# Kernel tuning notes

Hardware: AMD Instinct MI355X
Metric: run time of the kernel (lower is better)

## Reference

```python
import jax, jax.numpy as jnp
import numpy as np

B, L, D, T = 32, 512, 1024, 256
MAX_MENTION_LEN = 10
NEG_INF = float('-inf')


def _static_bounds_and_keep():
    # Full (start, end) grid, flattened row-major like torch's .view(-1, 2)
    s = np.repeat(np.arange(L), L)
    e = np.tile(np.arange(L), L)
    bounds = np.stack([s, e], axis=-1)            # [L*L, 2]
    keep = (e - s) <= MAX_MENTION_LEN             # static per-position mask
    idx = np.nonzero(keep)[0]
    return jnp.asarray(bounds[keep], jnp.int32), jnp.asarray(idx, jnp.int32)


def setup_inputs() -> dict:
    key = jax.random.key(0)
    k0, k1, k2 = jax.random.split(key, 3)
    text_encodings = jax.random.normal(k0, (B, L, D), dtype=jnp.float32)
    mask_ctxt = jnp.ones((B, L), dtype=jnp.int32)
    # word -> wordpiece mapping: [start, end_exclusive); values kept in [1, L)
    tokens_mapping = jax.random.randint(k1, (B, T, 2), 1, L).astype(jnp.int32)
    W = jax.random.normal(k2, (D, 3), dtype=jnp.float32) * 0.02
    b = jnp.zeros((3,), dtype=jnp.float32)
    return {"text_encodings": text_encodings, "mask_ctxt": mask_ctxt,
            "tokens_mapping": tokens_mapping, "W": W, "b": b}


def reference(text_encodings, mask_ctxt, tokens_mapping, W, b):
    # per-token start / end / mention logits
    logits = jnp.einsum('bld,dk->blk', text_encodings, W) + b  # [B, L, 3]
    valid_tok = (mask_ctxt == 1)
    start_lp = jnp.where(valid_tok, logits[:, :, 0], NEG_INF)
    end_lp = jnp.where(valid_tok, logits[:, :, 1], NEG_INF)
    mention_lp = jnp.where(valid_tok, logits[:, :, 2], NEG_INF)

    # scores[b, s, e] = start[b, s] + end[b, e] + sum_{i=s..e} mention[b, i]
    scores = start_lp[:, :, None] + end_lp[:, None, :]          # [B, L, L]
    csum = jnp.cumsum(mention_lp, axis=1)                        # [B, L]
    csum_prev = jnp.concatenate(
        [jnp.zeros((csum.shape[0], 1), csum.dtype), csum[:, :-1]], axis=1)
    scores = scores + (csum[:, None, :] - csum_prev[:, :, None])

    # mention_sizes > 0  <=>  e >= s
    pos = jnp.arange(L)
    size_ok = pos[None, :, None] <= pos[None, None, :]           # [1, L, L]

    # token-boundary masks (scatter 1 at word starts / ends, zero col 0)
    bidx = jnp.arange(tokens_mapping.shape[0])[:, None]
    ts = jnp.zeros(mask_ctxt.shape, jnp.int32).at[bidx, tokens_mapping[:, :, 0]].set(1)
    ts = ts.at[:, 0].set(0)
    te = jnp.zeros(mask_ctxt.shape, jnp.int32).at[bidx, tokens_mapping[:, :, 1] - 1].set(1)
    te = te.at[:, 0].set(0)
    vse = ts[:, :, None] * te[:, None, :]                        # bmm outer product

    valid = size_ok & (mask_ctxt[:, :, None] > 0) & (vse > 0)
    scores = jnp.where(valid, scores, NEG_INF)

    scores_flat = scores.reshape(scores.shape[0], -1)            # [B, L*L]
    bounds_keep, keep_idx = _static_bounds_and_keep()
    out_scores = scores_flat[:, keep_idx]                        # [B, K]
    out_bounds = jnp.broadcast_to(bounds_keep[None],
                                  (scores.shape[0],) + bounds_keep.shape)
    return out_scores, out_bounds
```

## Files before the change

kernel.cpp:

```cpp
#include <hip/hip_runtime.h>
#include <math.h>

#define BB 32
#define LL 512
#define DD 1024
#define TT 256
#define NK 136393
#define NK_LIN 131273
#define S_LIN 502
#define NEG_BIG  -3.0e38f
#define NEG_MASK -1.0e30f
#define P_TOT (BB * NK)
#define SC4 (P_TOT / 4)
#define MEMSET_BLOCKS ((SC4 + 255) / 256)
#define BCHUNKS ((NK + 255) / 256)
#define D1_BLOCKS (MEMSET_BLOCKS + 2 * BCHUNKS)
#define GEMV_BLOCKS (BB * LL / 4)

typedef float f4v __attribute__((ext_vector_type(4)));
typedef float f2v __attribute__((ext_vector_type(2)));

__device__ __forceinline__ int off_s(int s) {
    return (s <= S_LIN) ? s * (s + 21) / 2 : NK_LIN + (s - S_LIN) * LL;
}

__global__ __launch_bounds__(256) void write_kernel(float* __restrict__ out)
{
    const int id = blockIdx.x;
    const int t  = threadIdx.x;

    if (id < MEMSET_BLOCKS) {
        const int i = id * 256 + t;
        if (i < SC4) {
            f4v neg = {NEG_BIG, NEG_BIG, NEG_BIG, NEG_BIG};
            ((f4v*)out)[i] = neg;
        }
        return;
    }

    const int q = id - MEMSET_BLOCKS;
    const int g = (q >= BCHUNKS) ? 1 : 0;
    const int c = q - g * BCHUNKS;
    const int p = c * 256 + t;
    if (p >= NK) return;
    int s, e;
    if (p >= NK_LIN) {
        const int rr = p - NK_LIN;
        s = S_LIN + (rr >> 9);
        e = rr & 511;
    } else {
        float f = sqrtf(8.0f * (float)p + 441.0f);
        s = (int)((f - 21.0f) * 0.5f);
        if (s < 0) s = 0;
        if (s > 501) s = 501;
        while ((s + 1) * (s + 22) / 2 <= p) ++s;
        while (s * (s + 21) / 2 > p) --s;
        e = p - s * (s + 21) / 2;
    }
    f2v v = {(float)s, (float)e};
    f2v* bp = (f2v*)(out + (size_t)P_TOT);
#pragma unroll
    for (int j = 0; j < 16; ++j) {
        const int b = g * 16 + j;
        bp[(size_t)b * NK + p] = v;
    }
}

__global__ __launch_bounds__(256) void gemv_kernel(
    const float* __restrict__ text, const float* __restrict__ W,
    const float* __restrict__ bias, const int* __restrict__ mask,
    float* __restrict__ slp, float* __restrict__ elp, float* __restrict__ mlp)
{
    const int wid  = threadIdx.x >> 6;
    const int lane = threadIdx.x & 63;
    const int row  = blockIdx.x * 4 + wid;
    const f4v* t4 = (const f4v*)(text + (size_t)row * DD);
    const f4v* w4 = (const f4v*)W;
    float a0 = 0.f, a1 = 0.f, a2 = 0.f;
#pragma unroll
    for (int j = 0; j < 4; ++j) {
        const int fi = lane + j * 64;
        f4v v  = t4[fi];
        f4v w0 = w4[fi * 3 + 0];
        f4v w1 = w4[fi * 3 + 1];
        f4v w2 = w4[fi * 3 + 2];
        a0 += v.x * w0.x;  a1 += v.x * w0.y;  a2 += v.x * w0.z;
        a0 += v.y * w0.w;  a1 += v.y * w1.x;  a2 += v.y * w1.y;
        a0 += v.z * w1.z;  a1 += v.z * w1.w;  a2 += v.z * w2.x;
        a0 += v.w * w2.y;  a1 += v.w * w2.z;  a2 += v.w * w2.w;
    }
#pragma unroll
    for (int o = 32; o; o >>= 1) {
        a0 += __shfl_down(a0, o);
        a1 += __shfl_down(a1, o);
        a2 += __shfl_down(a2, o);
    }
    if (lane == 0) {
        const int m = mask[row];
        slp[row] = (m == 1) ? a0 + bias[0] : NEG_MASK;
        elp[row] = (m == 1) ? a1 + bias[1] : NEG_MASK;
        mlp[row] = (m == 1) ? a2 + bias[2] : NEG_MASK;
    }
}

__global__ __launch_bounds__(512) void tail_kernel(
    const float* __restrict__ slp, const float* __restrict__ elp,
    const float* __restrict__ mlp, const int* __restrict__ mask,
    const int* __restrict__ tmap, float* __restrict__ out)
{
    const int b = blockIdx.x;
    const int j = blockIdx.y;
    const int t = threadIdx.x;
    __shared__ float sl[LL], el[LL], ml[LL];
    __shared__ unsigned char tsl[LL], tel[LL];

    const int idx = b * LL + t;
    tsl[t] = 0; tel[t] = 0;
    sl[t] = slp[idx]; el[t] = elp[idx]; ml[t] = mlp[idx];
    __syncthreads();
    if (t < TT) {
        int s0 = tmap[((size_t)b * TT + t) * 2 + 0];
        int e0 = tmap[((size_t)b * TT + t) * 2 + 1] - 1;
        s0 = min(max(s0, 0), LL - 1);
        e0 = min(max(e0, 0), LL - 1);
        tsl[s0] = 1;
        tel[e0] = 1;
    }
    __syncthreads();

    const int s = t;
    const int e = s + j;
    if (s > 0 && e < LL && tsl[s] && tel[e] && mask[idx] == 1) {
        float w = 0.f;
        for (int l = s; l <= e; ++l) w += ml[l];
        float sc = sl[s] + el[e] + w;
        if (sc < -1.0e29f) sc = NEG_BIG;
        out[(size_t)b * NK + off_s(s) + e] = sc;
    }
}

extern "C" void kernel_launch(void* const* d_in, const int* in_sizes, int n_in,
                              void* d_out, int out_size, void* d_ws, size_t ws_size,
                              hipStream_t stream) {
    const float* text = (const float*)d_in[0];
    const int*   mask = (const int*)d_in[1];
    const int*   tmap = (const int*)d_in[2];
    const float* W    = (const float*)d_in[3];
    const float* bias = (const float*)d_in[4];
    float* out = (float*)d_out;

    float* slp = (float*)d_ws;
    float* elp = slp + (size_t)BB * LL;
    float* mlp = elp + (size_t)BB * LL;

    write_kernel<<<D1_BLOCKS, 256, 0, stream>>>(out);
    gemv_kernel<<<GEMV_BLOCKS, 256, 0, stream>>>(text, W, bias, mask,
                                                 slp, elp, mlp);
    dim3 g3(BB, 11);
    tail_kernel<<<g3, 512, 0, stream>>>(slp, elp, mlp, mask, tmap, out);
}
```

Before: 28.70 us.

## Fuse logit GEMV into span-scoring kernel with halo row recomputation

Drops the separate GEMV kernel and its workspace round trip. Each of 512 blocks now computes start, end and mention logits for its 32 start rows plus a 10-row halo, keeping them in shared memory and software-pipelining three row buffers per wave. Span scores for that window are then written directly. This saves a kernel launch and the global logits write/read, but reads and recomputes about 31% extra text rows at window boundaries. Those extra reads may partly hit in L2.

New measurement: 30.66 us. 1.07x slower.

```diff
diff --git a/kernel.cpp b/kernel.cpp
--- a/kernel.cpp
+++ b/kernel.cpp
@@ -15,7 +15,7 @@
 #define MEMSET_BLOCKS ((SC4 + 255) / 256)
 #define BCHUNKS ((NK + 255) / 256)
 #define D1_BLOCKS (MEMSET_BLOCKS + 2 * BCHUNKS)
-#define GEMV_BLOCKS (BB * LL / 4)
+#define TAIL_BLOCKS 512
 
 typedef float f4v __attribute__((ext_vector_type(4)));
 typedef float f2v __attribute__((ext_vector_type(2)));
@@ -66,76 +66,103 @@
     }
 }
 
-__global__ __launch_bounds__(256) void gemv_kernel(
+#define LOADR(buf, lr)                                                    \
+    if ((lr) < wlen) {                                                    \
+        const f4v* t4 = (const f4v*)(text + (size_t)(rowg0 + (lr)) * DD); \
+        _Pragma("unroll")                                                 \
+        for (int j = 0; j < 4; ++j) buf[j] = t4[lane + j * 64];           \
+    }
+
+#define REDUCER(buf, lr)                                                  \
+    if ((lr) < wlen) {                                                    \
+        float a0 = 0.f, a1 = 0.f, a2 = 0.f;                               \
+        _Pragma("unroll")                                                 \
+        for (int j = 0; j < 4; ++j) {                                     \
+            f4v v = buf[j];                                               \
+            f4v w0 = wr[j*3], w1 = wr[j*3+1], w2 = wr[j*3+2];             \
+            a0 += v.x * w0.x;  a1 += v.x * w0.y;  a2 += v.x * w0.z;       \
+            a0 += v.y * w0.w;  a1 += v.y * w1.x;  a2 += v.y * w1.y;       \
+            a0 += v.z * w1.z;  a1 += v.z * w1.w;  a2 += v.z * w2.x;       \
+            a0 += v.w * w2.y;  a1 += v.w * w2.z;  a2 += v.w * w2.w;       \
+        }                                                                 \
+        _Pragma("unroll")                                                 \
+        for (int o = 32; o; o >>= 1) {                                    \
+            a0 += __shfl_down(a0, o);                                     \
+            a1 += __shfl_down(a1, o);                                     \
+            a2 += __shfl_down(a2, o);                                     \
+        }                                                                 \
+        if (lane == 0) {                                                  \
+            const int m = mask[rowg0 + (lr)];                             \
+            sl[lr] = (m == 1) ? a0 + b0 : NEG_MASK;                       \
+            el[lr] = (m == 1) ? a1 + b1 : NEG_MASK;                       \
+            ml[lr] = (m == 1) ? a2 + b2 : NEG_MASK;                       \
+        }                                                                 \
+    }
+
+__global__ __launch_bounds__(512) void tail_kernel(
     const float* __restrict__ text, const float* __restrict__ W,
     const float* __restrict__ bias, const int* __restrict__ mask,
-    float* __restrict__ slp, float* __restrict__ elp, float* __restrict__ mlp)
+    const int* __restrict__ tmap, float* __restrict__ out)
 {
-    const int wid  = threadIdx.x >> 6;
-    const int lane = threadIdx.x & 63;
-    const int row  = blockIdx.x * 4 + wid;
-    const f4v* t4 = (const f4v*)(text + (size_t)row * DD);
+    const int q    = blockIdx.x;
+    const int b    = q >> 4;
+    const int r0   = (q & 15) << 5;
+    const int wlen = min(42, LL - r0);
+    const int rowg0 = b * LL + r0;
+    const int t    = threadIdx.x;
+    const int wid  = t >> 6, lane = t & 63;
+
+    __shared__ float sl[42], el[42], ml[42];
+    __shared__ unsigned char tsw[42], tew[42];
+
     const f4v* w4 = (const f4v*)W;
-    float a0 = 0.f, a1 = 0.f, a2 = 0.f;
+    f4v wr[12];
 #pragma unroll
     for (int j = 0; j < 4; ++j) {
         const int fi = lane + j * 64;
-        f4v v  = t4[fi];
-        f4v w0 = w4[fi * 3 + 0];
-        f4v w1 = w4[fi * 3 + 1];
-        f4v w2 = w4[fi * 3 + 2];
-        a0 += v.x * w0.x;  a1 += v.x * w0.y;  a2 += v.x * w0.z;
-        a0 += v.y * w0.w;  a1 += v.y * w1.x;  a2 += v.y * w1.y;
-        a0 += v.z * w1.z;  a1 += v.z * w1.w;  a2 += v.z * w2.x;
-        a0 += v.w * w2.y;  a1 += v.w * w2.z;  a2 += v.w * w2.w;
+        wr[j*3+0] = w4[fi*3+0]; wr[j*3+1] = w4[fi*3+1]; wr[j*3+2] = w4[fi*3+2];
     }
-#pragma unroll
-    for (int o = 32; o; o >>= 1) {
-        a0 += __shfl_down(a0, o);
-        a1 += __shfl_down(a1, o);
-        a2 += __shfl_down(a2, o);
-    }
-    if (lane == 0) {
-        const int m = mask[row];
-        slp[row] = (m == 1) ? a0 + bias[0] : NEG_MASK;
-        elp[row] = (m == 1) ? a1 + bias[1] : NEG_MASK;
-        mlp[row] = (m == 1) ? a2 + bias[2] : NEG_MASK;
-    }
-}
+    const float b0 = bias[0], b1 = bias[1], b2 = bias[2];
 
-__global__ __launch_bounds__(512) void tail_kernel(
-    const float* __restrict__ slp, const float* __restrict__ elp,
-    const float* __restrict__ mlp, const int* __restrict__ mask,
-    const int* __restrict__ tmap, float* __restrict__ out)
-{
-    const int b = blockIdx.x;
-    const int j = blockIdx.y;
-    const int t = threadIdx.x;
-    __shared__ float sl[LL], el[LL], ml[LL];
-    __shared__ unsigned char tsl[LL], tel[LL];
+    f4v bufA[4], bufB[4], bufC[4];
+    LOADR(bufA, wid);
+    LOADR(bufB, wid + 8);
+    LOADR(bufC, wid + 16);
+    REDUCER(bufA, wid);        LOADR(bufA, wid + 24);
+    REDUCER(bufB, wid + 8);    LOADR(bufB, wid + 32);
+    REDUCER(bufC, wid + 16);   LOADR(bufC, wid + 40);
+    REDUCER(bufA, wid + 24);
+    REDUCER(bufB, wid + 32);
+    REDUCER(bufC, wid + 40);
 
-    const int idx = b * LL + t;
-    tsl[t] = 0; tel[t] = 0;
-    sl[t] = slp[idx]; el[t] = elp[idx]; ml[t] = mlp[idx];
+    if (t < 42) { tsw[t] = 0; tew[t] = 0; }
     __syncthreads();
     if (t < TT) {
         int s0 = tmap[((size_t)b * TT + t) * 2 + 0];
         int e0 = tmap[((size_t)b * TT + t) * 2 + 1] - 1;
         s0 = min(max(s0, 0), LL - 1);
         e0 = min(max(e0, 0), LL - 1);
-        tsl[s0] = 1;
-        tel[e0] = 1;
+        if (s0 >= r0 && s0 < r0 + wlen) tsw[s0 - r0] = 1;
+        if (e0 >= r0 && e0 < r0 + wlen) tew[e0 - r0] = 1;
     }
     __syncthreads();
 
-    const int s = t;
-    const int e = s + j;
-    if (s > 0 && e < LL && tsl[s] && tel[e] && mask[idx] == 1) {
-        float w = 0.f;
-        for (int l = s; l <= e; ++l) w += ml[l];
-        float sc = sl[s] + el[e] + w;
-        if (sc < -1.0e29f) sc = NEG_BIG;
-        out[(size_t)b * NK + off_s(s) + e] = sc;
+    if (t < 32 * 11) {
+        const int s_loc = t / 11;
+        const int j     = t - s_loc * 11;
+        const int s     = r0 + s_loc;
+        const int e     = s + j;
+        if (e < LL) {
+            const int e_loc = s_loc + j;
+            float v = NEG_BIG;
+            if (s > 0 && tsw[s_loc] && tew[e_loc]) {
+                float w = 0.f;
+                for (int l = s_loc; l <= e_loc; ++l) w += ml[l];
+                v = sl[s_loc] + el[e_loc] + w;
+                if (v < -1.0e29f) v = NEG_BIG;
+            }
+            out[(size_t)b * NK + off_s(s) + e] = v;
+        }
     }
 }
 
@@ -149,13 +176,6 @@
     const float* bias = (const float*)d_in[4];
     float* out = (float*)d_out;
 
-    float* slp = (float*)d_ws;
-    float* elp = slp + (size_t)BB * LL;
-    float* mlp = elp + (size_t)BB * LL;
-
     write_kernel<<<D1_BLOCKS, 256, 0, stream>>>(out);
-    gemv_kernel<<<GEMV_BLOCKS, 256, 0, stream>>>(text, W, bias, mask,
-                                                 slp, elp, mlp);
-    dim3 g3(BB, 11);
-    tail_kernel<<<g3, 512, 0, stream>>>(slp, elp, mlp, mask, tmap, out);
+    tail_kernel<<<TAIL_BLOCKS, 512, 0, stream>>>(text, W, bias, mask, tmap, out);
 }
```

## Fuse NEG_INF memset and score scatter into one dense fill kernel

Applied to the files above, without the earlier changes.

Drops the separate pass that pre-fills the whole score buffer with -inf followed by a sparse scatter of valid scores. A single fill kernel now writes each output row once, computing either the score or -inf per element with vector stores. It splits the s-range into balanced per-batch segments so each block gets similar work. The bounds-writing work moves into the same launch, cutting one kernel launch and one full pass of writes over the score buffer. The cost is redundant per-element branching and a serial mention-sum loop done inside the fill.

Result: slower. 60.82 us (+111.9%).

```diff
diff --git a/kernel.cpp b/kernel.cpp
--- a/kernel.cpp
+++ b/kernel.cpp
@@ -11,59 +11,21 @@
 #define NEG_BIG  -3.0e38f
 #define NEG_MASK -1.0e30f
 #define P_TOT (BB * NK)
-#define SC4 (P_TOT / 4)
-#define MEMSET_BLOCKS ((SC4 + 255) / 256)
+#define GEMV_BLOCKS (BB * LL / 4)
+#define NSEG 16
+#define FILL_BLOCKS (BB * NSEG)
 #define BCHUNKS ((NK + 255) / 256)
-#define D1_BLOCKS (MEMSET_BLOCKS + 2 * BCHUNKS)
-#define GEMV_BLOCKS (BB * LL / 4)
+#define D2_BLOCKS (FILL_BLOCKS + 2 * BCHUNKS)
+#define MAXW 131
 
 typedef float f4v __attribute__((ext_vector_type(4)));
 typedef float f2v __attribute__((ext_vector_type(2)));
 
+__device__ __constant__ int d_splits[NSEG + 1] =
+    {0, 121, 175, 216, 251, 282, 310, 335, 359, 381, 403, 423, 442, 460, 478, 495, 512};
+
 __device__ __forceinline__ int off_s(int s) {
     return (s <= S_LIN) ? s * (s + 21) / 2 : NK_LIN + (s - S_LIN) * LL;
-}
-
-__global__ __launch_bounds__(256) void write_kernel(float* __restrict__ out)
-{
-    const int id = blockIdx.x;
-    const int t  = threadIdx.x;
-
-    if (id < MEMSET_BLOCKS) {
-        const int i = id * 256 + t;
-        if (i < SC4) {
-            f4v neg = {NEG_BIG, NEG_BIG, NEG_BIG, NEG_BIG};
-            ((f4v*)out)[i] = neg;
-        }
-        return;
-    }
-
-    const int q = id - MEMSET_BLOCKS;
-    const int g = (q >= BCHUNKS) ? 1 : 0;
-    const int c = q - g * BCHUNKS;
-    const int p = c * 256 + t;
-    if (p >= NK) return;
-    int s, e;
-    if (p >= NK_LIN) {
-        const int rr = p - NK_LIN;
-        s = S_LIN + (rr >> 9);
-        e = rr & 511;
-    } else {
-        float f = sqrtf(8.0f * (float)p + 441.0f);
-        s = (int)((f - 21.0f) * 0.5f);
-        if (s < 0) s = 0;
-        if (s > 501) s = 501;
-        while ((s + 1) * (s + 22) / 2 <= p) ++s;
-        while (s * (s + 21) / 2 > p) --s;
-        e = p - s * (s + 21) / 2;
-    }
-    f2v v = {(float)s, (float)e};
-    f2v* bp = (f2v*)(out + (size_t)P_TOT);
-#pragma unroll
-    for (int j = 0; j < 16; ++j) {
-        const int b = g * 16 + j;
-        bp[(size_t)b * NK + p] = v;
-    }
 }
 
 __global__ __launch_bounds__(256) void gemv_kernel(
@@ -103,39 +65,108 @@
     }
 }
 
-__global__ __launch_bounds__(512) void tail_kernel(
+__global__ __launch_bounds__(256) void fill_kernel(
     const float* __restrict__ slp, const float* __restrict__ elp,
-    const float* __restrict__ mlp, const int* __restrict__ mask,
-    const int* __restrict__ tmap, float* __restrict__ out)
+    const float* __restrict__ mlp, const int* __restrict__ tmap,
+    float* __restrict__ out)
 {
-    const int b = blockIdx.x;
-    const int j = blockIdx.y;
-    const int t = threadIdx.x;
-    __shared__ float sl[LL], el[LL], ml[LL];
-    __shared__ unsigned char tsl[LL], tel[LL];
+    const int id = blockIdx.x;
+    const int t  = threadIdx.x;
 
-    const int idx = b * LL + t;
-    tsl[t] = 0; tel[t] = 0;
-    sl[t] = slp[idx]; el[t] = elp[idx]; ml[t] = mlp[idx];
-    __syncthreads();
-    if (t < TT) {
-        int s0 = tmap[((size_t)b * TT + t) * 2 + 0];
-        int e0 = tmap[((size_t)b * TT + t) * 2 + 1] - 1;
-        s0 = min(max(s0, 0), LL - 1);
-        e0 = min(max(e0, 0), LL - 1);
-        tsl[s0] = 1;
-        tel[e0] = 1;
+    if (id < FILL_BLOCKS) {
+        const int b   = id >> 4;
+        const int seg = id & 15;
+        const int a   = d_splits[seg], bnd = d_splits[seg + 1];
+        const int wlen = min(bnd + 10, LL) - a;
+
+        __shared__ float sl[MAXW], el[MAXW], ml[MAXW];
+        __shared__ unsigned char tsw[MAXW], tew[MAXW];
+
+        for (int i = t; i < wlen; i += 256) {
+            const int row = b * LL + a + i;
+            sl[i] = slp[row]; el[i] = elp[row]; ml[i] = mlp[row];
+            tsw[i] = 0; tew[i] = 0;
+        }
+        __syncthreads();
+        if (t < TT) {
+            int s0 = tmap[((size_t)b * TT + t) * 2 + 0];
+            int e0 = tmap[((size_t)b * TT + t) * 2 + 1] - 1;
+            s0 = min(max(s0, 0), LL - 1);
+            e0 = min(max(e0, 0), LL - 1);
+            if (s0 >= a && s0 < a + wlen) tsw[s0 - a] = 1;
+            if (e0 >= a && e0 < a + wlen) tew[e0 - a] = 1;
+        }
+        __syncthreads();
+
+        const int wid = t >> 6, lane = t & 63;
+        const size_t bb = (size_t)b * NK;
+
+        for (int s = a + wid; s < bnd; s += 4) {
+            const int s_loc = s - a;
+            const int n = min(s + 11, LL);
+            const size_t rowbase = bb + off_s(s);
+
+            auto val = [&](int e) -> float {
+                if (e < s) return NEG_BIG;
+                float v = NEG_BIG;
+                if (s > 0 && tsw[s_loc] && tew[e - a]) {
+                    float w = 0.f;
+                    for (int l = s_loc; l <= e - a; ++l) w += ml[l];
+                    v = sl[s_loc] + el[e - a] + w;
+                    if (v < -1.0e29f) v = NEG_BIG;
+                }
+                return v;
+            };
+
+            const int head = (int)((4 - (rowbase & 3)) & 3);
+            const int hh = min(head, n);
+            if (lane < hh) out[rowbase + lane] = val(lane);
+            const int nb4 = (n - hh) >> 2;
+            for (int j = lane; j < nb4; j += 64) {
+                const int e0 = hh + 4 * j;
+                f4v v;
+                if (e0 + 3 < s) {
+                    v = (f4v){NEG_BIG, NEG_BIG, NEG_BIG, NEG_BIG};
+                } else {
+                    v.x = val(e0); v.y = val(e0 + 1);
+                    v.z = val(e0 + 2); v.w = val(e0 + 3);
+                }
+                *(f4v*)(out + rowbase + e0) = v;
+            }
+            const int rem = (n - hh) & 3;
+            if (lane < rem) {
+                const int e = hh + 4 * nb4 + lane;
+                out[rowbase + e] = val(e);
+            }
+        }
+        return;
     }
-    __syncthreads();
 
-    const int s = t;
-    const int e = s + j;
-    if (s > 0 && e < LL && tsl[s] && tel[e] && mask[idx] == 1) {
-        float w = 0.f;
-        for (int l = s; l <= e; ++l) w += ml[l];
-        float sc = sl[s] + el[e] + w;
-        if (sc < -1.0e29f) sc = NEG_BIG;
-        out[(size_t)b * NK + off_s(s) + e] = sc;
+    const int q = id - FILL_BLOCKS;
+    const int g = (q >= BCHUNKS) ? 1 : 0;
+    const int c = q - g * BCHUNKS;
+    const int p = c * 256 + t;
+    if (p >= NK) return;
+    int s, e;
+    if (p >= NK_LIN) {
+        const int rr = p - NK_LIN;
+        s = S_LIN + (rr >> 9);
+        e = rr & 511;
+    } else {
+        float f = sqrtf(8.0f * (float)p + 441.0f);
+        s = (int)((f - 21.0f) * 0.5f);
+        if (s < 0) s = 0;
+        if (s > 501) s = 501;
+        while ((s + 1) * (s + 22) / 2 <= p) ++s;
+        while (s * (s + 21) / 2 > p) --s;
+        e = p - s * (s + 21) / 2;
+    }
+    f2v v = {(float)s, (float)e};
+    f2v* bp = (f2v*)(out + (size_t)P_TOT);
+#pragma unroll
+    for (int j = 0; j < 16; ++j) {
+        const int b = g * 16 + j;
+        bp[(size_t)b * NK + p] = v;
     }
 }
 
@@ -153,9 +184,7 @@
     float* elp = slp + (size_t)BB * LL;
     float* mlp = elp + (size_t)BB * LL;
 
-    write_kernel<<<D1_BLOCKS, 256, 0, stream>>>(out);
     gemv_kernel<<<GEMV_BLOCKS, 256, 0, stream>>>(text, W, bias, mask,
                                                  slp, elp, mlp);
-    dim3 g3(BB, 11);
-    tail_kernel<<<g3, 512, 0, stream>>>(slp, elp, mlp, mask, tmap, out);
+    fill_kernel<<<D2_BLOCKS, 256, 0, stream>>>(slp, elp, mlp, tmap, out);
 }
```

## Merge memset, bounds and score emission into one kernel and skip redundant fills

Applied to the files above, without the earlier changes.

The separate write kernel is folded into the post-GEMV emit kernel, giving two launches instead of three. The NEG_INF fill now skips positions the tail blocks write themselves (e >= s), so each output word is stored once rather than memset and then overwritten. Tail blocks now write NEG_BIG explicitly for invalid in-band entries. The mask check is dropped from the tail, and masked rows still come out NEG_BIG through the logit threshold. The cost is per-thread index inversion (sqrt plus loops) in the memset path, and the fill and bounds writes can no longer overlap the GEMV.

New measurement: 27.72 us. -3.4%, faster.

```diff
diff --git a/kernel.cpp b/kernel.cpp
--- a/kernel.cpp
+++ b/kernel.cpp
@@ -12,10 +12,11 @@
 #define NEG_MASK -1.0e30f
 #define P_TOT (BB * NK)
 #define SC4 (P_TOT / 4)
-#define MEMSET_BLOCKS ((SC4 + 255) / 256)
+#define GEMV_BLOCKS (BB * LL / 4)
+#define TAIL_CNT (BB * 11)
+#define MEMSET_CNT ((SC4 + 255) / 256)
 #define BCHUNKS ((NK + 255) / 256)
-#define D1_BLOCKS (MEMSET_BLOCKS + 2 * BCHUNKS)
-#define GEMV_BLOCKS (BB * LL / 4)
+#define D2_BLOCKS (TAIL_CNT + MEMSET_CNT + 2 * BCHUNKS)
 
 typedef float f4v __attribute__((ext_vector_type(4)));
 typedef float f2v __attribute__((ext_vector_type(2)));
@@ -23,46 +24,19 @@
 __device__ __forceinline__ int off_s(int s) {
     return (s <= S_LIN) ? s * (s + 21) / 2 : NK_LIN + (s - S_LIN) * LL;
 }
-
-__global__ __launch_bounds__(256) void write_kernel(float* __restrict__ out)
-{
-    const int id = blockIdx.x;
-    const int t  = threadIdx.x;
-
-    if (id < MEMSET_BLOCKS) {
-        const int i = id * 256 + t;
-        if (i < SC4) {
-            f4v neg = {NEG_BIG, NEG_BIG, NEG_BIG, NEG_BIG};
-            ((f4v*)out)[i] = neg;
-        }
-        return;
-    }
-
-    const int q = id - MEMSET_BLOCKS;
-    const int g = (q >= BCHUNKS) ? 1 : 0;
-    const int c = q - g * BCHUNKS;
-    const int p = c * 256 + t;
-    if (p >= NK) return;
-    int s, e;
-    if (p >= NK_LIN) {
-        const int rr = p - NK_LIN;
-        s = S_LIN + (rr >> 9);
-        e = rr & 511;
+__device__ __forceinline__ void invert(int k, int& s, int& e) {
+    if (k >= NK_LIN) {
+        const int r = k - NK_LIN;
+        s = S_LIN + (r >> 9);
+        e = r & 511;
     } else {
-        float f = sqrtf(8.0f * (float)p + 441.0f);
+        float f = sqrtf(8.0f * (float)k + 441.0f);
         s = (int)((f - 21.0f) * 0.5f);
         if (s < 0) s = 0;
         if (s > 501) s = 501;
-        while ((s + 1) * (s + 22) / 2 <= p) ++s;
-        while (s * (s + 21) / 2 > p) --s;
-        e = p - s * (s + 21) / 2;
-    }
-    f2v v = {(float)s, (float)e};
-    f2v* bp = (f2v*)(out + (size_t)P_TOT);
-#pragma unroll
-    for (int j = 0; j < 16; ++j) {
-        const int b = g * 16 + j;
-        bp[(size_t)b * NK + p] = v;
+        while ((s + 1) * (s + 22) / 2 <= k) ++s;
+        while (s * (s + 21) / 2 > k) --s;
+        e = k - s * (s + 21) / 2;
     }
 }
 
@@ -103,39 +77,94 @@
     }
 }
 
-__global__ __launch_bounds__(512) void tail_kernel(
+__global__ __launch_bounds__(256) void emit_kernel(
     const float* __restrict__ slp, const float* __restrict__ elp,
-    const float* __restrict__ mlp, const int* __restrict__ mask,
-    const int* __restrict__ tmap, float* __restrict__ out)
+    const float* __restrict__ mlp, const int* __restrict__ tmap,
+    float* __restrict__ out)
 {
-    const int b = blockIdx.x;
-    const int j = blockIdx.y;
-    const int t = threadIdx.x;
-    __shared__ float sl[LL], el[LL], ml[LL];
-    __shared__ unsigned char tsl[LL], tel[LL];
+    const int id = blockIdx.x;
+    const int t  = threadIdx.x;
 
-    const int idx = b * LL + t;
-    tsl[t] = 0; tel[t] = 0;
-    sl[t] = slp[idx]; el[t] = elp[idx]; ml[t] = mlp[idx];
-    __syncthreads();
-    if (t < TT) {
-        int s0 = tmap[((size_t)b * TT + t) * 2 + 0];
-        int e0 = tmap[((size_t)b * TT + t) * 2 + 1] - 1;
-        s0 = min(max(s0, 0), LL - 1);
-        e0 = min(max(e0, 0), LL - 1);
-        tsl[s0] = 1;
-        tel[e0] = 1;
+    if (id < TAIL_CNT) {
+        const int b = id / 11;
+        const int j = id - b * 11;
+        __shared__ float sl[LL], el[LL], ml[LL];
+        __shared__ unsigned char tsl[LL], tel[LL];
+        const int base = b * LL;
+#pragma unroll
+        for (int h = 0; h < 2; ++h) {
+            const int i = t + h * 256;
+            sl[i] = slp[base + i]; el[i] = elp[base + i]; ml[i] = mlp[base + i];
+            tsl[i] = 0; tel[i] = 0;
+        }
+        __syncthreads();
+        if (t < TT) {
+            int s0 = tmap[((size_t)b * TT + t) * 2 + 0];
+            int e0 = tmap[((size_t)b * TT + t) * 2 + 1] - 1;
+            s0 = min(max(s0, 0), LL - 1);
+            e0 = min(max(e0, 0), LL - 1);
+            tsl[s0] = 1;
+            tel[e0] = 1;
+        }
+        __syncthreads();
+#pragma unroll
+        for (int h = 0; h < 2; ++h) {
+            const int s = t + h * 256;
+            const int e = s + j;
+            if (e < LL) {
+                float v = NEG_BIG;
+                if (s > 0 && tsl[s] && tel[e]) {
+                    float w = 0.f;
+                    for (int l = s; l <= e; ++l) w += ml[l];
+                    v = sl[s] + el[e] + w;
+                    if (v < -1.0e29f) v = NEG_BIG;
+                }
+                out[(size_t)b * NK + off_s(s) + e] = v;
+            }
+        }
+        return;
     }
-    __syncthreads();
 
-    const int s = t;
-    const int e = s + j;
-    if (s > 0 && e < LL && tsl[s] && tel[e] && mask[idx] == 1) {
-        float w = 0.f;
-        for (int l = s; l <= e; ++l) w += ml[l];
-        float sc = sl[s] + el[e] + w;
-        if (sc < -1.0e29f) sc = NEG_BIG;
-        out[(size_t)b * NK + off_s(s) + e] = sc;
+    if (id < TAIL_CNT + MEMSET_CNT) {
+        const int gid = (id - TAIL_CNT) * 256 + t;
+        if (gid >= SC4) return;
+        const int p4 = gid * 4;
+        const int b  = p4 / NK;
+        const int k  = p4 - b * NK;
+        int s, e;
+        invert(k, s, e);
+        if (e + 3 < s) {
+            f4v neg = {NEG_BIG, NEG_BIG, NEG_BIG, NEG_BIG};
+            *(f4v*)(out + p4) = neg;
+        } else {
+            int rowlen = (s <= S_LIN) ? (s + 11) : LL;
+#pragma unroll
+            for (int kk = 0; kk < 4; ++kk) {
+                if (e < s) out[p4 + kk] = NEG_BIG;
+                ++e;
+                if (e >= rowlen) {
+                    e = 0; ++s;
+                    if (s >= LL) s = 0;
+                    rowlen = (s <= S_LIN) ? (s + 11) : LL;
+                }
+            }
+        }
+        return;
+    }
+
+    const int q = id - TAIL_CNT - MEMSET_CNT;
+    const int g = (q >= BCHUNKS) ? 1 : 0;
+    const int c = q - g * BCHUNKS;
+    const int p = c * 256 + t;
+    if (p >= NK) return;
+    int s, e;
+    invert(p, s, e);
+    f2v v = {(float)s, (float)e};
+    f2v* bp = (f2v*)(out + (size_t)P_TOT);
+#pragma unroll
+    for (int j = 0; j < 16; ++j) {
+        const int b = g * 16 + j;
+        bp[(size_t)b * NK + p] = v;
     }
 }
 
@@ -153,9 +182,7 @@
     float* elp = slp + (size_t)BB * LL;
     float* mlp = elp + (size_t)BB * LL;
 
-    write_kernel<<<D1_BLOCKS, 256, 0, stream>>>(out);
     gemv_kernel<<<GEMV_BLOCKS, 256, 0, stream>>>(text, W, bias, mask,
                                                  slp, elp, mlp);
-    dim3 g3(BB, 11);
-    tail_kernel<<<g3, 512, 0, stream>>>(slp, elp, mlp, mask, tmap, out);
+    emit_kernel<<<D2_BLOCKS, 256, 0, stream>>>(slp, elp, mlp, tmap, out);
 }
```
